# Performance work log

Hardware: AMD Instinct MI355X
Metric: run time of the kernel (lower is better)

The kernel has to match this reference:

```python
import jax, jax.numpy as jnp
import numpy as np


def setup_inputs() -> dict:
    key = jax.random.key(0)
    ks = jax.random.split(key, 8)
    B, N, D, Fn, Fe = 16, 512, 64, 32, 1
    return {
        "prev_embeddings": jax.random.normal(ks[0], (B, N, D), dtype=jnp.float32),
        "adj": jax.random.uniform(ks[1], (B, N, N), dtype=jnp.float32),
        "node_features": jax.random.normal(ks[2], (B, N, Fn), dtype=jnp.float32),
        "edge_features": jax.random.uniform(ks[3], (B, N, N), dtype=jnp.float32),
        "W1": jax.random.normal(ks[4], (Fn, D), dtype=jnp.float32) * (1.0 / np.sqrt(Fn)),
        "W2": jax.random.normal(ks[5], (D, D), dtype=jnp.float32) * (1.0 / np.sqrt(D)),
        "W3": jax.random.normal(ks[6], (D, D), dtype=jnp.float32) * (1.0 / np.sqrt(D)),
        "W4": jax.random.normal(ks[7], (Fe, D), dtype=jnp.float32),
    }


def reference(prev_embeddings, adj, node_features, edge_features, W1, W2, W3, W4):
    # x1 = theta1(node_features): (B,N,D)
    x1 = jnp.einsum("bnf,fd->bnd", node_features, W1)
    # x2 = theta2(adj @ prev): (B,N,D)
    x2 = jnp.einsum("bij,bjd,de->bie", adj, prev_embeddings, W2)
    # edge_features (B,N,N) -> (B,N,N,1); x4 = relu(theta4(e)): (B,N,N,D)
    e = edge_features[..., None]
    x4 = jax.nn.relu(jnp.einsum("bijf,fd->bijd", e, W4))
    # adjacency-weighted sum over neighbors j: (B,N,D)
    s = jnp.einsum("bij,bijd->bid", adj, x4)
    x3 = jnp.einsum("bid,de->bie", s, W3)
    return jax.nn.relu(x1 + x2 + x3)
```

## Files before the change

### kernel.cpp

```cpp
#include <hip/hip_runtime.h>

#define NN 512
#define DD 64
#define FN 32
#define NROWS 8192

typedef unsigned short ushortT;
typedef __attribute__((ext_vector_type(4))) unsigned short us4;
typedef __attribute__((ext_vector_type(8))) short s8;
typedef __attribute__((ext_vector_type(4))) float f4;

__device__ inline ushortT f2bf(float x) {
    unsigned u = __float_as_uint(x);
    return (ushortT)((u + 0x7FFFu + ((u >> 16) & 1u)) >> 16);
}

__global__ __launch_bounds__(256) void prep_kernel(
    const float* __restrict__ prev, const float* __restrict__ adj,
    const float* __restrict__ nf,   const float* __restrict__ ef,
    const float* __restrict__ W1,   const float* __restrict__ W2,
    const float* __restrict__ W3,   const float* __restrict__ W4,
    ushortT* __restrict__ adjb, ushortT* __restrict__ prevT,
    ushortT* __restrict__ nfb,  ushortT* __restrict__ W1T,
    ushortT* __restrict__ W2T,  float* __restrict__ v3,
    float* __restrict__ tbuf)
{
    const int bk = blockIdx.x, tid = threadIdx.x;

    if (bk < 512) {
        const int lane = tid & 63, w = tid >> 6;
        const int row0 = bk * 16 + w * 4;
        #pragma unroll
        for (int r = 0; r < 4; ++r) {
            const int row = row0 + r;
            const float4* a4 = (const float4*)(adj + row * NN);
            const float4* e4 = (const float4*)(ef  + row * NN);
            float4 a0 = a4[lane], a1 = a4[64 + lane];
            float4 e0 = e4[lane], e1 = e4[64 + lane];
            float tp = a0.x*e0.x + a0.y*e0.y + a0.z*e0.z + a0.w*e0.w
                     + a1.x*e1.x + a1.y*e1.y + a1.z*e1.z + a1.w*e1.w;
            #pragma unroll
            for (int s = 1; s < 64; s <<= 1) tp += __shfl_xor(tp, s, 64);
            us4 o0 = { f2bf(a0.x), f2bf(a0.y), f2bf(a0.z), f2bf(a0.w) };
            us4 o1 = { f2bf(a1.x), f2bf(a1.y), f2bf(a1.z), f2bf(a1.w) };
            ((us4*)(adjb + row * NN))[lane]      = o0;
            ((us4*)(adjb + row * NN))[64 + lane] = o1;
            if (lane == 0) tbuf[row] = tp;
        }
    } else if (bk < 528) {
        __shared__ float T[64][65];
        const int b = bk - 512;
        for (int c = 0; c < 8; ++c) {
            #pragma unroll
            for (int s = 0; s < 16; ++s) {
                int idx = s * 256 + tid;
                int jl = idx >> 6, d = idx & 63;
                T[jl][d] = prev[b * NN * DD + (c * 64 + jl) * DD + d];
            }
            __syncthreads();
            #pragma unroll
            for (int s = 0; s < 16; ++s) {
                int idx = s * 256 + tid;
                int d = idx >> 6, jl = idx & 63;
                prevT[b * DD * NN + d * NN + c * 64 + jl] = f2bf(T[jl][d]);
            }
            __syncthreads();
        }
    } else if (bk < 592) {
        const int base = (bk - 528) * 4096;
        #pragma unroll
        for (int s = 0; s < 4; ++s) {
            int i = base + s * 1024 + tid * 4;
            float4 v = *(const float4*)(nf + i);
            us4 o = { f2bf(v.x), f2bf(v.y), f2bf(v.z), f2bf(v.w) };
            *(us4*)(nfb + i) = o;
        }
    } else {
        for (int i = tid; i < DD * FN; i += 256) {
            int e = i >> 5, f = i & 31;
            W1T[i] = f2bf(W1[f * DD + e]);
        }
        for (int i = tid; i < DD * DD; i += 256) {
            int e = i >> 6, d = i & 63;
            W2T[i] = f2bf(W2[d * DD + e]);
        }
        if (tid < DD) {
            float s = 0.f;
            for (int d = 0; d < DD; ++d)
                s = fmaf(fmaxf(W4[d], 0.f), W3[d * DD + tid], s);
            v3[tid] = s;
        }
    }
}

__global__ __launch_bounds__(64) void gemm_kernel(
    const ushortT* __restrict__ adjb, const ushortT* __restrict__ prevT,
    const ushortT* __restrict__ nfb,  const ushortT* __restrict__ W1T,
    const ushortT* __restrict__ W2T,  const float* __restrict__ v3,
    const float* __restrict__ tbuf,   float* __restrict__ out)
{
    __shared__ __align__(16) ushortT PT[16 * 72];

    const int l   = threadIdx.x;
    const int i0  = blockIdx.x * 16;
    const int b   = i0 >> 9;
    const int l15 = l & 15, g = l >> 4;

    f4 zero = {0.f, 0.f, 0.f, 0.f};
    f4 acc[4] = {zero, zero, zero, zero};
    const ushortT* arow = adjb  + (i0 + l15) * NN + 8 * g;
    const ushortT* pb   = prevT + b * DD * NN + l15 * NN + 8 * g;

    #pragma unroll
    for (int ks = 0; ks < 16; ++ks) {
        s8 A = *(const s8*)(arow + 32 * ks);
        #pragma unroll
        for (int nt = 0; nt < 4; ++nt) {
            s8 B = *(const s8*)(pb + nt * 16 * NN + 32 * ks);
            acc[nt] = __builtin_amdgcn_mfma_f32_16x16x32_bf16(A, B, acc[nt], 0, 0, 0);
        }
    }

    #pragma unroll
    for (int nt = 0; nt < 4; ++nt)
        #pragma unroll
        for (int r = 0; r < 4; ++r)
            PT[(4 * g + r) * 72 + 16 * nt + l15] = f2bf(acc[nt][r]);

    float tr[4];
    #pragma unroll
    for (int r = 0; r < 4; ++r) tr[r] = tbuf[i0 + 4 * g + r];
    f4 o[4];
    #pragma unroll
    for (int nt = 0; nt < 4; ++nt) {
        float vv = v3[16 * nt + l15];
        o[nt][0] = tr[0] * vv; o[nt][1] = tr[1] * vv;
        o[nt][2] = tr[2] * vv; o[nt][3] = tr[3] * vv;
    }

    s8 A1 = *(const s8*)(nfb + (i0 + l15) * FN + 8 * g);
    #pragma unroll
    for (int nt = 0; nt < 4; ++nt) {
        s8 B1 = *(const s8*)(W1T + (16 * nt + l15) * FN + 8 * g);
        o[nt] = __builtin_amdgcn_mfma_f32_16x16x32_bf16(A1, B1, o[nt], 0, 0, 0);
    }

    #pragma unroll
    for (int k2 = 0; k2 < 2; ++k2) {
        s8 A2 = *(const s8*)(&PT[l15 * 72 + 32 * k2 + 8 * g]);
        #pragma unroll
        for (int nt = 0; nt < 4; ++nt) {
            s8 B2 = *(const s8*)(W2T + (16 * nt + l15) * DD + 32 * k2 + 8 * g);
            o[nt] = __builtin_amdgcn_mfma_f32_16x16x32_bf16(A2, B2, o[nt], 0, 0, 0);
        }
    }

    float* orow = out + i0 * DD;
    #pragma unroll
    for (int nt = 0; nt < 4; ++nt)
        #pragma unroll
        for (int r = 0; r < 4; ++r)
            orow[(4 * g + r) * DD + 16 * nt + l15] = fmaxf(o[nt][r], 0.f);
}

extern "C" void kernel_launch(void* const* d_in, const int* in_sizes, int n_in,
                              void* d_out, int out_size, void* d_ws, size_t ws_size,
                              hipStream_t stream) {
    const float* prev = (const float*)d_in[0];
    const float* adj  = (const float*)d_in[1];
    const float* nf   = (const float*)d_in[2];
    const float* ef   = (const float*)d_in[3];
    const float* W1   = (const float*)d_in[4];
    const float* W2   = (const float*)d_in[5];
    const float* W3   = (const float*)d_in[6];
    const float* W4   = (const float*)d_in[7];
    float* out = (float*)d_out;

    char* ws = (char*)d_ws;
    ushortT* adjb  = (ushortT*)(ws + 0);
    ushortT* prevT = (ushortT*)(ws + 8388608);
    ushortT* nfb   = (ushortT*)(ws + 9437184);
    ushortT* W1T   = (ushortT*)(ws + 9961472);
    ushortT* W2T   = (ushortT*)(ws + 9965568);
    float*   v3    = (float*)  (ws + 9973760);
    float*   tbuf  = (float*)  (ws + 9974016);

    prep_kernel<<<dim3(593), dim3(256), 0, stream>>>(
        prev, adj, nf, ef, W1, W2, W3, W4, adjb, prevT, nfb, W1T, W2T, v3, tbuf);
    gemm_kernel<<<dim3(512), dim3(64), 0, stream>>>(
        adjb, prevT, nfb, W1T, W2T, v3, tbuf, out);
}
```

Baseline: 102.3 us.

## Fuse adj bf16 conversion and edge reduction into GEMM with split-K across waves

```diff
diff --git a/kernel.cpp b/kernel.cpp
--- a/kernel.cpp
+++ b/kernel.cpp
@@ -3,7 +3,6 @@
 #define NN 512
 #define DD 64
 #define FN 32
-#define NROWS 8192
 
 typedef unsigned short ushortT;
 typedef __attribute__((ext_vector_type(4))) unsigned short us4;
@@ -16,40 +15,18 @@
 }
 
 __global__ __launch_bounds__(256) void prep_kernel(
-    const float* __restrict__ prev, const float* __restrict__ adj,
-    const float* __restrict__ nf,   const float* __restrict__ ef,
+    const float* __restrict__ prev, const float* __restrict__ nf,
     const float* __restrict__ W1,   const float* __restrict__ W2,
     const float* __restrict__ W3,   const float* __restrict__ W4,
-    ushortT* __restrict__ adjb, ushortT* __restrict__ prevT,
-    ushortT* __restrict__ nfb,  ushortT* __restrict__ W1T,
-    ushortT* __restrict__ W2T,  float* __restrict__ v3,
-    float* __restrict__ tbuf)
+    ushortT* __restrict__ prevT, ushortT* __restrict__ nfb,
+    ushortT* __restrict__ W1T,   ushortT* __restrict__ W2T,
+    float* __restrict__ v3)
 {
     const int bk = blockIdx.x, tid = threadIdx.x;
 
-    if (bk < 512) {
-        const int lane = tid & 63, w = tid >> 6;
-        const int row0 = bk * 16 + w * 4;
-        #pragma unroll
-        for (int r = 0; r < 4; ++r) {
-            const int row = row0 + r;
-            const float4* a4 = (const float4*)(adj + row * NN);
-            const float4* e4 = (const float4*)(ef  + row * NN);
-            float4 a0 = a4[lane], a1 = a4[64 + lane];
-            float4 e0 = e4[lane], e1 = e4[64 + lane];
-            float tp = a0.x*e0.x + a0.y*e0.y + a0.z*e0.z + a0.w*e0.w
-                     + a1.x*e1.x + a1.y*e1.y + a1.z*e1.z + a1.w*e1.w;
-            #pragma unroll
-            for (int s = 1; s < 64; s <<= 1) tp += __shfl_xor(tp, s, 64);
-            us4 o0 = { f2bf(a0.x), f2bf(a0.y), f2bf(a0.z), f2bf(a0.w) };
-            us4 o1 = { f2bf(a1.x), f2bf(a1.y), f2bf(a1.z), f2bf(a1.w) };
-            ((us4*)(adjb + row * NN))[lane]      = o0;
-            ((us4*)(adjb + row * NN))[64 + lane] = o1;
-            if (lane == 0) tbuf[row] = tp;
-        }
-    } else if (bk < 528) {
+    if (bk < 16) {
         __shared__ float T[64][65];
-        const int b = bk - 512;
+        const int b = bk;
         for (int c = 0; c < 8; ++c) {
             #pragma unroll
             for (int s = 0; s < 16; ++s) {
@@ -66,8 +43,8 @@
             }
             __syncthreads();
         }
-    } else if (bk < 592) {
-        const int base = (bk - 528) * 4096;
+    } else if (bk < 80) {
+        const int base = (bk - 16) * 4096;
         #pragma unroll
         for (int s = 0; s < 4; ++s) {
             int i = base + s * 1024 + tid * 4;
@@ -93,30 +70,51 @@
     }
 }
 
-__global__ __launch_bounds__(64) void gemm_kernel(
-    const ushortT* __restrict__ adjb, const ushortT* __restrict__ prevT,
-    const ushortT* __restrict__ nfb,  const ushortT* __restrict__ W1T,
-    const ushortT* __restrict__ W2T,  const float* __restrict__ v3,
-    const float* __restrict__ tbuf,   float* __restrict__ out)
+#define APITCH 136
+#define CPITCH 68
+__global__ __launch_bounds__(256) void gemm_kernel(
+    const float* __restrict__ adj,   const float* __restrict__ ef,
+    const ushortT* __restrict__ prevT, const ushortT* __restrict__ nfb,
+    const ushortT* __restrict__ W1T, const ushortT* __restrict__ W2T,
+    const float* __restrict__ v3,    float* __restrict__ out)
 {
+    __shared__ __align__(16) ushortT adjS[4 * 16 * APITCH];
+    __shared__ __align__(16) float   Cpart[4 * 16 * CPITCH];
     __shared__ __align__(16) ushortT PT[16 * 72];
+    __shared__ float tpart[4][16];
+    __shared__ float tsum[16];
 
-    const int l   = threadIdx.x;
-    const int i0  = blockIdx.x * 16;
-    const int b   = i0 >> 9;
-    const int l15 = l & 15, g = l >> 4;
+    const int tid  = threadIdx.x;
+    const int lane = tid & 63;
+    const int w    = __builtin_amdgcn_readfirstlane(tid >> 6);
+    const int i0   = blockIdx.x * 16;
+    const int b    = blockIdx.x >> 5;
+    const int l15  = lane & 15, g = lane >> 4;
+    const int l31  = lane & 31, half = lane >> 5;
+
+    #pragma unroll
+    for (int it = 0; it < 8; ++it) {
+        const int r = 2 * it + half;
+        const float4* a4 = (const float4*)(adj + (i0 + r) * NN + 128 * w);
+        const float4* e4 = (const float4*)(ef  + (i0 + r) * NN + 128 * w);
+        float4 av = a4[l31], ev = e4[l31];
+        float tp = av.x*ev.x + av.y*ev.y + av.z*ev.z + av.w*ev.w;
+        #pragma unroll
+        for (int s = 1; s < 32; s <<= 1) tp += __shfl_xor(tp, s, 64);
+        if (l31 == 0) tpart[w][r] = tp;
+        us4 ov = { f2bf(av.x), f2bf(av.y), f2bf(av.z), f2bf(av.w) };
+        *(us4*)(&adjS[w * 16 * APITCH + r * APITCH + 4 * l31]) = ov;
+    }
 
     f4 zero = {0.f, 0.f, 0.f, 0.f};
     f4 acc[4] = {zero, zero, zero, zero};
-    const ushortT* arow = adjb  + (i0 + l15) * NN + 8 * g;
-    const ushortT* pb   = prevT + b * DD * NN + l15 * NN + 8 * g;
-
+    const ushortT* pb = prevT + b * DD * NN + l15 * NN + 128 * w + 8 * g;
     #pragma unroll
-    for (int ks = 0; ks < 16; ++ks) {
-        s8 A = *(const s8*)(arow + 32 * ks);
+    for (int ksl = 0; ksl < 4; ++ksl) {
+        s8 A = *(const s8*)(&adjS[w * 16 * APITCH + l15 * APITCH + 32 * ksl + 8 * g]);
         #pragma unroll
         for (int nt = 0; nt < 4; ++nt) {
-            s8 B = *(const s8*)(pb + nt * 16 * NN + 32 * ks);
+            s8 B = *(const s8*)(pb + nt * 16 * NN + 32 * ksl);
             acc[nt] = __builtin_amdgcn_mfma_f32_16x16x32_bf16(A, B, acc[nt], 0, 0, 0);
         }
     }
@@ -125,42 +123,46 @@
     for (int nt = 0; nt < 4; ++nt)
         #pragma unroll
         for (int r = 0; r < 4; ++r)
-            PT[(4 * g + r) * 72 + 16 * nt + l15] = f2bf(acc[nt][r]);
+            Cpart[w * 16 * CPITCH + (4 * g + r) * CPITCH + 16 * nt + l15] = acc[nt][r];
+    __syncthreads();
 
-    float tr[4];
+    {
+        const int row = tid >> 4, c0 = (tid & 15) * 4;
+        us4 o;
+        #pragma unroll
+        for (int c = 0; c < 4; ++c) {
+            float s = Cpart[0 * 16 * CPITCH + row * CPITCH + c0 + c]
+                    + Cpart[1 * 16 * CPITCH + row * CPITCH + c0 + c]
+                    + Cpart[2 * 16 * CPITCH + row * CPITCH + c0 + c]
+                    + Cpart[3 * 16 * CPITCH + row * CPITCH + c0 + c];
+            o[c] = f2bf(s);
+        }
+        *(us4*)(&PT[row * 72 + c0]) = o;
+        if (tid < 16)
+            tsum[tid] = tpart[0][tid] + tpart[1][tid] + tpart[2][tid] + tpart[3][tid];
+    }
+    __syncthreads();
+
+    float vv = v3[16 * w + l15];
+    f4 o;
     #pragma unroll
-    for (int r = 0; r < 4; ++r) tr[r] = tbuf[i0 + 4 * g + r];
-    f4 o[4];
-    #pragma unroll
-    for (int nt = 0; nt < 4; ++nt) {
-        float vv = v3[16 * nt + l15];
-        o[nt][0] = tr[0] * vv; o[nt][1] = tr[1] * vv;
-        o[nt][2] = tr[2] * vv; o[nt][3] = tr[3] * vv;
-    }
+    for (int r = 0; r < 4; ++r) o[r] = tsum[4 * g + r] * vv;
 
     s8 A1 = *(const s8*)(nfb + (i0 + l15) * FN + 8 * g);
-    #pragma unroll
-    for (int nt = 0; nt < 4; ++nt) {
-        s8 B1 = *(const s8*)(W1T + (16 * nt + l15) * FN + 8 * g);
-        o[nt] = __builtin_amdgcn_mfma_f32_16x16x32_bf16(A1, B1, o[nt], 0, 0, 0);
-    }
+    s8 B1 = *(const s8*)(W1T + (16 * w + l15) * FN + 8 * g);
+    o = __builtin_amdgcn_mfma_f32_16x16x32_bf16(A1, B1, o, 0, 0, 0);
 
     #pragma unroll
     for (int k2 = 0; k2 < 2; ++k2) {
         s8 A2 = *(const s8*)(&PT[l15 * 72 + 32 * k2 + 8 * g]);
-        #pragma unroll
-        for (int nt = 0; nt < 4; ++nt) {
-            s8 B2 = *(const s8*)(W2T + (16 * nt + l15) * DD + 32 * k2 + 8 * g);
-            o[nt] = __builtin_amdgcn_mfma_f32_16x16x32_bf16(A2, B2, o[nt], 0, 0, 0);
-        }
+        s8 B2 = *(const s8*)(W2T + (16 * w + l15) * DD + 32 * k2 + 8 * g);
+        o = __builtin_amdgcn_mfma_f32_16x16x32_bf16(A2, B2, o, 0, 0, 0);
     }
 
     float* orow = out + i0 * DD;
     #pragma unroll
-    for (int nt = 0; nt < 4; ++nt)
-        #pragma unroll
-        for (int r = 0; r < 4; ++r)
-            orow[(4 * g + r) * DD + 16 * nt + l15] = fmaxf(o[nt][r], 0.f);
+    for (int r = 0; r < 4; ++r)
+        orow[(4 * g + r) * DD + 16 * w + l15] = fmaxf(o[r], 0.f);
 }
 
 extern "C" void kernel_launch(void* const* d_in, const int* in_sizes, int n_in,
@@ -177,16 +179,14 @@
     float* out = (float*)d_out;
 
     char* ws = (char*)d_ws;
-    ushortT* adjb  = (ushortT*)(ws + 0);
-    ushortT* prevT = (ushortT*)(ws + 8388608);
-    ushortT* nfb   = (ushortT*)(ws + 9437184);
-    ushortT* W1T   = (ushortT*)(ws + 9961472);
-    ushortT* W2T   = (ushortT*)(ws + 9965568);
-    float*   v3    = (float*)  (ws + 9973760);
-    float*   tbuf  = (float*)  (ws + 9974016);
+    ushortT* prevT = (ushortT*)(ws + 0);
+    ushortT* nfb   = (ushortT*)(ws + 1048576);
+    ushortT* W1T   = (ushortT*)(ws + 1572864);
+    ushortT* W2T   = (ushortT*)(ws + 1576960);
+    float*   v3    = (float*)  (ws + 1585152);
 
-    prep_kernel<<<dim3(593), dim3(256), 0, stream>>>(
-        prev, adj, nf, ef, W1, W2, W3, W4, adjb, prevT, nfb, W1T, W2T, v3, tbuf);
-    gemm_kernel<<<dim3(512), dim3(64), 0, stream>>>(
-        adjb, prevT, nfb, W1T, W2T, v3, tbuf, out);
+    prep_kernel<<<dim3(81), dim3(256), 0, stream>>>(
+        prev, nf, W1, W2, W3, W4, prevT, nfb, W1T, W2T, v3);
+    gemm_kernel<<<dim3(512), dim3(256), 0, stream>>>(
+        adj, ef, prevT, nfb, W1T, W2T, v3, out);
 }
```

Result: no change. 101.9 us (-0.4%).
